# Performance work log

Hardware: AMD Instinct MI355X
Metric: run time of the kernel (lower is better)

The kernel has to match this reference:

```python
import jax, jax.numpy as jnp
import numpy as np


def _bilinear_sample(fea, gx, gy):
    """grid_sample, bilinear, zero padding, align_corners=True.
    fea: [B,C,H,W]; gx, gy: [B,N] normalized coords in [-1,1]. Returns [B,N,C]."""
    B, C, H, W = fea.shape
    feaT = fea.transpose(0, 2, 3, 1)  # [B,H,W,C]
    x = (gx + 1.0) * ((W - 1) * 0.5)
    y = (gy + 1.0) * ((H - 1) * 0.5)
    x0 = jnp.floor(x)
    y0 = jnp.floor(y)
    bidx = jnp.arange(B)[:, None]
    out = jnp.zeros(gx.shape + (C,), fea.dtype)
    for dx, dy in ((0, 0), (1, 0), (0, 1), (1, 1)):
        xi = x0 + dx
        yi = y0 + dy
        w = (1.0 - jnp.abs(x - xi)) * (1.0 - jnp.abs(y - yi))
        valid = (xi >= 0) & (xi <= W - 1) & (yi >= 0) & (yi <= H - 1)
        xic = jnp.clip(xi, 0, W - 1).astype(jnp.int32)
        yic = jnp.clip(yi, 0, H - 1).astype(jnp.int32)
        vals = feaT[bidx, yic, xic]  # [B,N,C]
        out = out + (w * valid.astype(fea.dtype))[:, :, None] * vals
    return out


def _homo_warping(src_fea, src_proj, ref_proj, depth_values):
    """src_fea [B,C,H,W]; src_proj/ref_proj [B,4,4]; depth_values [B,D,H,W].
    Returns warped volume [B,C,D,H,W]."""
    B, C, H, W = src_fea.shape
    D = depth_values.shape[1]
    proj = jnp.einsum('bij,bjk->bik', src_proj, jnp.linalg.inv(ref_proj))
    rot = proj[:, :3, :3]
    trans = proj[:, :3, 3]
    ys, xs = jnp.meshgrid(jnp.arange(H, dtype=src_fea.dtype),
                          jnp.arange(W, dtype=src_fea.dtype), indexing='ij')
    xyz = jnp.stack([xs.ravel(), ys.ravel(), jnp.ones(H * W, src_fea.dtype)], 0)  # [3,HW]
    rot_xyz = jnp.einsum('bij,jn->bin', rot, xyz)  # [B,3,HW]
    d = depth_values.reshape(B, 1, D, H * W)
    pxyz = rot_xyz[:, :, None, :] * d + trans[:, :, None, None]  # [B,3,D,HW]
    z = pxyz[:, 2]
    gx = pxyz[:, 0] / z
    gy = pxyz[:, 1] / z
    nx = gx / ((W - 1) * 0.5) - 1.0
    ny = gy / ((H - 1) * 0.5) - 1.0
    sampled = _bilinear_sample(src_fea, nx.reshape(B, -1), ny.reshape(B, -1))  # [B,D*H*W,C]
    return sampled.reshape(B, D, H, W, C).transpose(0, 4, 1, 2, 3)


def _combine_proj(proj):
    """proj [B,2,4,4]: [:,0]=extrinsic 4x4, [:,1,:3,:3]=intrinsic. Returns [B,4,4]."""
    upd = jnp.einsum('bij,bjk->bik', proj[:, 1, :3, :3], proj[:, 0, :3, :4])
    return proj[:, 0].at[:, :3, :4].set(upd)


def setup_inputs() -> dict:
    B, V, C, H, W, D = 2, 5, 32, 256, 320, 4
    key = jax.random.key(0)
    feats = jax.random.normal(key, (B, V, C, H, W), dtype=jnp.float32)
    rng = np.random.default_rng(0)
    K = np.eye(4, dtype=np.float32)
    K[0, 0] = 0.9 * W; K[1, 1] = 0.9 * W; K[0, 2] = W / 2.0; K[1, 2] = H / 2.0
    projs = np.zeros((B, V, 2, 4, 4), dtype=np.float32)
    for b in range(B):
        for v in range(V):
            ang = 0.0 if v == 0 else float(rng.uniform(-0.05, 0.05))
            ca, sa = np.cos(ang), np.sin(ang)
            E = np.eye(4, dtype=np.float32)
            E[:3, :3] = np.array([[ca, 0, sa], [0, 1, 0], [-sa, 0, ca]], dtype=np.float32)
            if v > 0:
                E[:3, 3] = rng.uniform(-20, 20, size=3).astype(np.float32)
            projs[b, v, 0] = E
            projs[b, v, 1] = K
    dmin, dmax = 425.0, 935.0
    base = np.linspace(dmin, dmax, D, dtype=np.float32)
    depth = np.broadcast_to(base[None, :, None, None], (B, D, H, W)).copy()
    depth += rng.uniform(-5, 5, size=(B, D, H, W)).astype(np.float32)
    return {'feats': feats,
            'proj_matrices': jnp.asarray(projs),
            'depth_values': jnp.asarray(depth)}


def reference(feats, proj_matrices, depth_values):
    """HAMMER.get_volume_variance_and_mask.
    feats [B,V,C,H,W], proj_matrices [B,V,2,4,4], depth_values [B,D,H,W].
    Returns (volume_variance [B,C,D,H,W], cv_mask [B,H,W])."""
    B, V, C, H, W = feats.shape
    D = depth_values.shape[1]
    ref_proj = _combine_proj(proj_matrices[:, 0])
    ref_vol = jnp.broadcast_to(feats[:, 0, :, None], (B, C, D, H, W))
    vol_sum = ref_vol
    vol_sq = ref_vol ** 2
    cv_mask = jnp.zeros((B, H, W), feats.dtype)
    for v in range(1, V):
        src_proj = _combine_proj(proj_matrices[:, v])
        warped = _homo_warping(feats[:, v], src_proj, ref_proj, depth_values)
        cv_mask = cv_mask + jnp.count_nonzero(
            jnp.count_nonzero(warped, axis=1), axis=1).astype(feats.dtype)
        vol_sum = vol_sum + warped
        vol_sq = vol_sq + warped ** 2
    inv_v = 1.0 / V
    volume_variance = vol_sq * inv_v - (vol_sum * inv_v) ** 2
    return volume_variance, cv_mask
```

## Files before the change

kernel.cpp:

```cpp
#include <hip/hip_runtime.h>

constexpr int B = 2, V = 5, C = 32, H = 256, W = 320, D = 4;
constexpr int HW = H * W;

__device__ float g_rt[B * (V - 1) * 12];

__device__ void combine_np(const float* __restrict__ proj, int b, int v, float Mo[4][4]) {
    const float* E = proj + ((size_t)(b * V + v) * 2 + 0) * 16;
    const float* K = proj + ((size_t)(b * V + v) * 2 + 1) * 16;
    for (int i = 0; i < 3; i++)
        for (int j = 0; j < 4; j++) {
            float acc = __fadd_rn(0.0f, __fmul_rn(K[i * 4 + 0], E[0 * 4 + j]));
            acc = __fadd_rn(acc, __fmul_rn(K[i * 4 + 1], E[1 * 4 + j]));
            acc = __fadd_rn(acc, __fmul_rn(K[i * 4 + 2], E[2 * 4 + j]));
            Mo[i][j] = acc;
        }
    for (int j = 0; j < 4; j++) Mo[3][j] = E[3 * 4 + j];
}

__global__ void setup_proj(const float* __restrict__ proj) {
    int t = threadIdx.x;
    if (t >= B * (V - 1)) return;
    int b = t / (V - 1);
    int v = t % (V - 1) + 1;

    float R[4][4], S[4][4];
    combine_np(proj, b, 0, R);
    combine_np(proj, b, v, S);

    float I4[4][4];
    for (int i = 0; i < 4; i++)
        for (int j = 0; j < 4; j++) I4[i][j] = 0.0f;

    float d0 = __fdiv_rn(1.0f, R[0][0]);
    I4[0][0] = d0;
    float d1 = __fdiv_rn(1.0f, R[1][1]);
    I4[1][1] = d1;
    {
        float x0 = R[0][1];
        if (x0 != 0.0f) x0 = __fmul_rn(x0, I4[0][0]);
        I4[0][1] = __fmul_rn(x0, -d1);
    }
    float d2 = __fdiv_rn(1.0f, R[2][2]);
    I4[2][2] = d2;
    {
        float x0 = R[0][2], x1 = R[1][2];
        if (x0 != 0.0f) x0 = __fmul_rn(x0, I4[0][0]);
        if (x1 != 0.0f) {
            x0 = __fadd_rn(x0, __fmul_rn(x1, I4[0][1]));
            x1 = __fmul_rn(x1, I4[1][1]);
        }
        I4[0][2] = __fmul_rn(x0, -d2);
        I4[1][2] = __fmul_rn(x1, -d2);
    }
    float d3 = __fdiv_rn(1.0f, R[3][3]);
    I4[3][3] = d3;
    {
        float x0 = R[0][3], x1 = R[1][3], x2 = R[2][3];
        if (x0 != 0.0f) x0 = __fmul_rn(x0, I4[0][0]);
        if (x1 != 0.0f) {
            x0 = __fadd_rn(x0, __fmul_rn(x1, I4[0][1]));
            x1 = __fmul_rn(x1, I4[1][1]);
        }
        if (x2 != 0.0f) {
            x0 = __fadd_rn(x0, __fmul_rn(x2, I4[0][2]));
            x1 = __fadd_rn(x1, __fmul_rn(x2, I4[1][2]));
            x2 = __fmul_rn(x2, I4[2][2]);
        }
        I4[0][3] = __fmul_rn(x0, -d3);
        I4[1][3] = __fmul_rn(x1, -d3);
        I4[2][3] = __fmul_rn(x2, -d3);
    }

    float P[3][4];
    for (int i = 0; i < 3; i++)
        for (int k = 0; k < 4; k++) {
            float acc = 0.0f;
            for (int j = 0; j < 4; j++)
                acc = __fadd_rn(acc, __fmul_rn(S[i][j], I4[j][k]));
            P[i][k] = acc;
        }

    float* out = g_rt + t * 12;
    out[0] = P[0][0]; out[1] = P[0][1]; out[2] = P[0][2];
    out[3] = P[1][0]; out[4] = P[1][1]; out[5] = P[1][2];
    out[6] = P[2][0]; out[7] = P[2][1]; out[8] = P[2][2];
    out[9] = P[0][3]; out[10] = P[1][3]; out[11] = P[2][3];
}

__global__ __launch_bounds__(256) void warp_var(
    const float* __restrict__ feats,
    const float* __restrict__ depthv,
    float* __restrict__ var_out,
    float* __restrict__ mask_out)
{
    int idx = blockIdx.x * 256 + threadIdx.x;
    int w = idx % W;
    int h = (idx / W) % H;
    int d = (idx / HW) % D;
    int b = idx / (HW * D);

    float depth = depthv[idx];

    const float xf = (float)w, yf = (float)h;
    const float hwX = 0.5f * (float)(W - 1);
    const float hwY = 0.5f * (float)(H - 1);
    const float rcpX = 1.0f / 159.5f;
    const float rcpY = 1.0f / 127.5f;

    int   toff[V - 1][4];
    float twt[V - 1][4];

#pragma unroll
    for (int v = 1; v < V; v++) {
        const float* P = g_rt + ((size_t)b * (V - 1) + (v - 1)) * 12;
        float rx = __fadd_rn(__fmaf_rn(P[1], yf, __fmul_rn(P[0], xf)), P[2]);
        float ry = __fadd_rn(__fmaf_rn(P[4], yf, __fmul_rn(P[3], xf)), P[5]);
        float rz = __fadd_rn(__fmaf_rn(P[7], yf, __fmul_rn(P[6], xf)), P[8]);
        float px = __fadd_rn(__fmul_rn(rx, depth), P[9]);
        float py = __fadd_rn(__fmul_rn(ry, depth), P[10]);
        float pz = __fadd_rn(__fmul_rn(rz, depth), P[11]);
        float gx = __fdiv_rn(px, pz);
        float gy = __fdiv_rn(py, pz);
        float nx = __fadd_rn(__fmul_rn(gx, rcpX), -1.0f);
        float ny = __fadd_rn(__fmul_rn(gy, rcpY), -1.0f);
        float x = __fmul_rn(__fadd_rn(nx, 1.0f), hwX);
        float y = __fmul_rn(__fadd_rn(ny, 1.0f), hwY);

        float x0 = floorf(x), y0 = floorf(y);
        float x1 = x0 + 1.0f, y1 = y0 + 1.0f;

        float wx0 = __fadd_rn(1.0f, -fabsf(__fadd_rn(x, -x0)));
        float wx1 = __fadd_rn(1.0f, -fabsf(__fadd_rn(x, -x1)));
        float wy0 = __fadd_rn(1.0f, -fabsf(__fadd_rn(y, -y0)));
        float wy1 = __fadd_rn(1.0f, -fabsf(__fadd_rn(y, -y1)));

        float vx0 = (x0 >= 0.0f && x0 <= (float)(W - 1)) ? 1.0f : 0.0f;
        float vx1 = (x1 >= 0.0f && x1 <= (float)(W - 1)) ? 1.0f : 0.0f;
        float vy0 = (y0 >= 0.0f && y0 <= (float)(H - 1)) ? 1.0f : 0.0f;
        float vy1 = (y1 >= 0.0f && y1 <= (float)(H - 1)) ? 1.0f : 0.0f;

        float s00 = __fmul_rn(__fmul_rn(wx0, wy0), __fmul_rn(vx0, vy0));
        float s10 = __fmul_rn(__fmul_rn(wx1, wy0), __fmul_rn(vx1, vy0));
        float s01 = __fmul_rn(__fmul_rn(wx0, wy1), __fmul_rn(vx0, vy1));
        float s11 = __fmul_rn(__fmul_rn(wx1, wy1), __fmul_rn(vx1, vy1));

        int xi0 = (int)fminf(fmaxf(x0, 0.0f), (float)(W - 1));
        int xi1 = (int)fminf(fmaxf(x1, 0.0f), (float)(W - 1));
        int yi0 = (int)fminf(fmaxf(y0, 0.0f), (float)(H - 1));
        int yi1 = (int)fminf(fmaxf(y1, 0.0f), (float)(H - 1));

        int vb = (b * V + v) * C * HW;
        toff[v - 1][0] = vb + yi0 * W + xi0;
        toff[v - 1][1] = vb + yi0 * W + xi1;
        toff[v - 1][2] = vb + yi1 * W + xi0;
        toff[v - 1][3] = vb + yi1 * W + xi1;
        twt[v - 1][0] = s00;
        twt[v - 1][1] = s10;
        twt[v - 1][2] = s01;
        twt[v - 1][3] = s11;
    }

    const int rb = b * V * C * HW + h * W + w;
    const float inv_v = 1.0f / (float)V;
    const size_t obase = ((size_t)b * C * D + d) * HW + (size_t)h * W + w;

    int nzmask = 0;

#pragma unroll 2
    for (int c = 0; c < C; c++) {
        const int cofs = c * HW;
        float rv = feats[rb + cofs];
        float s = rv;
        float q = rv * rv;
#pragma unroll
        for (int v = 0; v < V - 1; v++) {
            float f00 = feats[toff[v][0] + cofs];
            float f10 = feats[toff[v][1] + cofs];
            float f01 = feats[toff[v][2] + cofs];
            float f11 = feats[toff[v][3] + cofs];
            float val = twt[v][0] * f00 + twt[v][1] * f10 + twt[v][2] * f01 + twt[v][3] * f11;
            nzmask |= (val != 0.0f) ? (1 << v) : 0;
            s += val;
            q += val * val;
        }
        float sm = s * inv_v;
        float vv = q * inv_v - sm * sm;
        __builtin_nontemporal_store(vv, &var_out[obase + (size_t)c * (D * HW)]);
    }

    float maskc = (float)__popc(nzmask);
    atomicAdd(&mask_out[(size_t)b * HW + (size_t)h * W + w], maskc);
}

extern "C" void kernel_launch(void* const* d_in, const int* in_sizes, int n_in,
                              void* d_out, int out_size, void* d_ws, size_t ws_size,
                              hipStream_t stream) {
    const float* feats = (const float*)d_in[0];
    const float* proj = (const float*)d_in[1];
    const float* depthv = (const float*)d_in[2];

    float* var = (float*)d_out;
    float* mask = var + (size_t)B * C * D * HW;

    hipMemsetAsync(mask, 0, sizeof(float) * (size_t)B * HW, stream);

    setup_proj<<<1, 64, 0, stream>>>(proj);

    int n = B * D * HW;
    warp_var<<<n / 256, 256, 0, stream>>>(feats, depthv, var, mask);
}
```

Before: 277.7 us.

## Process all depth planes per thread and drop mask atomics

Each thread now handles one pixel across all depth hypotheses, so the reference feature value is loaded once per channel instead of once per depth. The mask is computed fully per thread and written directly, which removes the memset and the atomic adds. Block size drops to 128 and a block-index swizzle is added. Per-thread register state grows sharply because offsets and weights are kept for all view-depth pairs, which risks spills and lower occupancy.

```diff
diff --git a/kernel.cpp b/kernel.cpp
--- a/kernel.cpp
+++ b/kernel.cpp
@@ -2,6 +2,9 @@
 
 constexpr int B = 2, V = 5, C = 32, H = 256, W = 320, D = 4;
 constexpr int HW = H * W;
+constexpr int NTHREAD = B * HW;
+constexpr int BLK = 128;
+constexpr int NBLK = NTHREAD / BLK;
 
 __device__ float g_rt[B * (V - 1) * 12];
 
@@ -88,19 +91,25 @@
     out[9] = P[0][3]; out[10] = P[1][3]; out[11] = P[2][3];
 }
 
-__global__ __launch_bounds__(256) void warp_var(
+__global__ __launch_bounds__(BLK, 2) void warp_var(
     const float* __restrict__ feats,
     const float* __restrict__ depthv,
     float* __restrict__ var_out,
     float* __restrict__ mask_out)
 {
-    int idx = blockIdx.x * 256 + threadIdx.x;
-    int w = idx % W;
-    int h = (idx / W) % H;
-    int d = (idx / HW) % D;
-    int b = idx / (HW * D);
-
-    float depth = depthv[idx];
+    int bid = blockIdx.x;
+    int bswz = (bid & 7) * (NBLK / 8) + (bid >> 3);
+    int idx = bswz * BLK + threadIdx.x;
+
+    int hw = idx % HW;
+    int b = idx / HW;
+    int w = hw % W;
+    int h = hw / W;
+
+    float dep[D];
+#pragma unroll
+    for (int d = 0; d < D; d++)
+        dep[d] = depthv[(size_t)(b * D + d) * HW + hw];
 
     const float xf = (float)w, yf = (float)h;
     const float hwX = 0.5f * (float)(W - 1);
@@ -108,8 +117,8 @@
     const float rcpX = 1.0f / 159.5f;
     const float rcpY = 1.0f / 127.5f;
 
-    int   toff[V - 1][4];
-    float twt[V - 1][4];
+    int   toff[(V - 1) * D][4];
+    float twt[(V - 1) * D][4];
 
 #pragma unroll
     for (int v = 1; v < V; v++) {
@@ -117,80 +126,90 @@
         float rx = __fadd_rn(__fmaf_rn(P[1], yf, __fmul_rn(P[0], xf)), P[2]);
         float ry = __fadd_rn(__fmaf_rn(P[4], yf, __fmul_rn(P[3], xf)), P[5]);
         float rz = __fadd_rn(__fmaf_rn(P[7], yf, __fmul_rn(P[6], xf)), P[8]);
-        float px = __fadd_rn(__fmul_rn(rx, depth), P[9]);
-        float py = __fadd_rn(__fmul_rn(ry, depth), P[10]);
-        float pz = __fadd_rn(__fmul_rn(rz, depth), P[11]);
-        float gx = __fdiv_rn(px, pz);
-        float gy = __fdiv_rn(py, pz);
-        float nx = __fadd_rn(__fmul_rn(gx, rcpX), -1.0f);
-        float ny = __fadd_rn(__fmul_rn(gy, rcpY), -1.0f);
-        float x = __fmul_rn(__fadd_rn(nx, 1.0f), hwX);
-        float y = __fmul_rn(__fadd_rn(ny, 1.0f), hwY);
-
-        float x0 = floorf(x), y0 = floorf(y);
-        float x1 = x0 + 1.0f, y1 = y0 + 1.0f;
-
-        float wx0 = __fadd_rn(1.0f, -fabsf(__fadd_rn(x, -x0)));
-        float wx1 = __fadd_rn(1.0f, -fabsf(__fadd_rn(x, -x1)));
-        float wy0 = __fadd_rn(1.0f, -fabsf(__fadd_rn(y, -y0)));
-        float wy1 = __fadd_rn(1.0f, -fabsf(__fadd_rn(y, -y1)));
-
-        float vx0 = (x0 >= 0.0f && x0 <= (float)(W - 1)) ? 1.0f : 0.0f;
-        float vx1 = (x1 >= 0.0f && x1 <= (float)(W - 1)) ? 1.0f : 0.0f;
-        float vy0 = (y0 >= 0.0f && y0 <= (float)(H - 1)) ? 1.0f : 0.0f;
-        float vy1 = (y1 >= 0.0f && y1 <= (float)(H - 1)) ? 1.0f : 0.0f;
-
-        float s00 = __fmul_rn(__fmul_rn(wx0, wy0), __fmul_rn(vx0, vy0));
-        float s10 = __fmul_rn(__fmul_rn(wx1, wy0), __fmul_rn(vx1, vy0));
-        float s01 = __fmul_rn(__fmul_rn(wx0, wy1), __fmul_rn(vx0, vy1));
-        float s11 = __fmul_rn(__fmul_rn(wx1, wy1), __fmul_rn(vx1, vy1));
-
-        int xi0 = (int)fminf(fmaxf(x0, 0.0f), (float)(W - 1));
-        int xi1 = (int)fminf(fmaxf(x1, 0.0f), (float)(W - 1));
-        int yi0 = (int)fminf(fmaxf(y0, 0.0f), (float)(H - 1));
-        int yi1 = (int)fminf(fmaxf(y1, 0.0f), (float)(H - 1));
-
-        int vb = (b * V + v) * C * HW;
-        toff[v - 1][0] = vb + yi0 * W + xi0;
-        toff[v - 1][1] = vb + yi0 * W + xi1;
-        toff[v - 1][2] = vb + yi1 * W + xi0;
-        toff[v - 1][3] = vb + yi1 * W + xi1;
-        twt[v - 1][0] = s00;
-        twt[v - 1][1] = s10;
-        twt[v - 1][2] = s01;
-        twt[v - 1][3] = s11;
-    }
-
-    const int rb = b * V * C * HW + h * W + w;
+        const int vb = (b * V + v) * C * HW;
+#pragma unroll
+        for (int d = 0; d < D; d++) {
+            const int p = (v - 1) * D + d;
+            float px = __fadd_rn(__fmul_rn(rx, dep[d]), P[9]);
+            float py = __fadd_rn(__fmul_rn(ry, dep[d]), P[10]);
+            float pz = __fadd_rn(__fmul_rn(rz, dep[d]), P[11]);
+            float gx = __fdiv_rn(px, pz);
+            float gy = __fdiv_rn(py, pz);
+            float nx = __fadd_rn(__fmul_rn(gx, rcpX), -1.0f);
+            float ny = __fadd_rn(__fmul_rn(gy, rcpY), -1.0f);
+            float x = __fmul_rn(__fadd_rn(nx, 1.0f), hwX);
+            float y = __fmul_rn(__fadd_rn(ny, 1.0f), hwY);
+
+            float x0 = floorf(x), y0 = floorf(y);
+            float x1 = x0 + 1.0f, y1 = y0 + 1.0f;
+
+            float wx0 = __fadd_rn(1.0f, -fabsf(__fadd_rn(x, -x0)));
+            float wx1 = __fadd_rn(1.0f, -fabsf(__fadd_rn(x, -x1)));
+            float wy0 = __fadd_rn(1.0f, -fabsf(__fadd_rn(y, -y0)));
+            float wy1 = __fadd_rn(1.0f, -fabsf(__fadd_rn(y, -y1)));
+
+            float vx0 = (x0 >= 0.0f && x0 <= (float)(W - 1)) ? 1.0f : 0.0f;
+            float vx1 = (x1 >= 0.0f && x1 <= (float)(W - 1)) ? 1.0f : 0.0f;
+            float vy0 = (y0 >= 0.0f && y0 <= (float)(H - 1)) ? 1.0f : 0.0f;
+            float vy1 = (y1 >= 0.0f && y1 <= (float)(H - 1)) ? 1.0f : 0.0f;
+
+            twt[p][0] = __fmul_rn(__fmul_rn(wx0, wy0), __fmul_rn(vx0, vy0));
+            twt[p][1] = __fmul_rn(__fmul_rn(wx1, wy0), __fmul_rn(vx1, vy0));
+            twt[p][2] = __fmul_rn(__fmul_rn(wx0, wy1), __fmul_rn(vx0, vy1));
+            twt[p][3] = __fmul_rn(__fmul_rn(wx1, wy1), __fmul_rn(vx1, vy1));
+
+            int xi0 = (int)fminf(fmaxf(x0, 0.0f), (float)(W - 1));
+            int xi1 = (int)fminf(fmaxf(x1, 0.0f), (float)(W - 1));
+            int yi0 = (int)fminf(fmaxf(y0, 0.0f), (float)(H - 1));
+            int yi1 = (int)fminf(fmaxf(y1, 0.0f), (float)(H - 1));
+
+            toff[p][0] = vb + yi0 * W + xi0;
+            toff[p][1] = vb + yi0 * W + xi1;
+            toff[p][2] = vb + yi1 * W + xi0;
+            toff[p][3] = vb + yi1 * W + xi1;
+        }
+    }
+
+    const int rb = b * V * C * HW + hw;
     const float inv_v = 1.0f / (float)V;
-    const size_t obase = ((size_t)b * C * D + d) * HW + (size_t)h * W + w;
+    const size_t obase = (size_t)b * C * D * HW + (size_t)hw;
 
     int nzmask = 0;
 
-#pragma unroll 2
     for (int c = 0; c < C; c++) {
         const int cofs = c * HW;
         float rv = feats[rb + cofs];
-        float s = rv;
-        float q = rv * rv;
+        float s[D], q[D];
+#pragma unroll
+        for (int d = 0; d < D; d++) {
+            s[d] = rv;
+            q[d] = rv * rv;
+        }
 #pragma unroll
         for (int v = 0; v < V - 1; v++) {
-            float f00 = feats[toff[v][0] + cofs];
-            float f10 = feats[toff[v][1] + cofs];
-            float f01 = feats[toff[v][2] + cofs];
-            float f11 = feats[toff[v][3] + cofs];
-            float val = twt[v][0] * f00 + twt[v][1] * f10 + twt[v][2] * f01 + twt[v][3] * f11;
-            nzmask |= (val != 0.0f) ? (1 << v) : 0;
-            s += val;
-            q += val * val;
-        }
-        float sm = s * inv_v;
-        float vv = q * inv_v - sm * sm;
-        __builtin_nontemporal_store(vv, &var_out[obase + (size_t)c * (D * HW)]);
-    }
-
-    float maskc = (float)__popc(nzmask);
-    atomicAdd(&mask_out[(size_t)b * HW + (size_t)h * W + w], maskc);
+#pragma unroll
+            for (int d = 0; d < D; d++) {
+                const int p = v * D + d;
+                float f00 = feats[toff[p][0] + cofs];
+                float f10 = feats[toff[p][1] + cofs];
+                float f01 = feats[toff[p][2] + cofs];
+                float f11 = feats[toff[p][3] + cofs];
+                float val = twt[p][0] * f00 + twt[p][1] * f10 + twt[p][2] * f01 + twt[p][3] * f11;
+                nzmask |= (val != 0.0f) ? (1 << p) : 0;
+                s[d] += val;
+                q[d] += val * val;
+            }
+        }
+#pragma unroll
+        for (int d = 0; d < D; d++) {
+            float sm = s[d] * inv_v;
+            float vv = q[d] * inv_v - sm * sm;
+            __builtin_nontemporal_store(
+                vv, &var_out[obase + (size_t)c * (D * HW) + (size_t)d * HW]);
+        }
+    }
+
+    mask_out[(size_t)b * HW + hw] = (float)__popc(nzmask);
 }
 
 extern "C" void kernel_launch(void* const* d_in, const int* in_sizes, int n_in,
@@ -203,10 +222,7 @@
     float* var = (float*)d_out;
     float* mask = var + (size_t)B * C * D * HW;
 
-    hipMemsetAsync(mask, 0, sizeof(float) * (size_t)B * HW, stream);
-
     setup_proj<<<1, 64, 0, stream>>>(proj);
 
-    int n = B * D * HW;
-    warp_var<<<n / 256, 256, 0, stream>>>(feats, depthv, var, mask);
-}
+    warp_var<<<NBLK, BLK, 0, stream>>>(feats, depthv, var, mask);
+}
```

Measured after the change: 299.5 us. +7.9%, slower.

## Interleave depth planes per thread group, swizzle blocks, reduce mask via shuffles

Applied to the files above, without the earlier changes.

Changes the thread-to-work mapping so that the four depth samples of each pixel sit in adjacent lanes, and remaps block IDs with a swizzle over eight groups. The per-pixel count mask is then reduced across the four lanes with shuffles and written directly. This removes the atomics and the memset launch. Adjacent lanes now share reference-feature loads and likely nearby gather addresses. The cost is that output stores and depth loads become strided across the four lanes instead of fully coalesced.

```diff
diff --git a/kernel.cpp b/kernel.cpp
--- a/kernel.cpp
+++ b/kernel.cpp
@@ -2,6 +2,9 @@
 
 constexpr int B = 2, V = 5, C = 32, H = 256, W = 320, D = 4;
 constexpr int HW = H * W;
+constexpr int NTHREAD = B * HW * D;
+constexpr int BLK = 256;
+constexpr int NBLK = NTHREAD / BLK;
 
 __device__ float g_rt[B * (V - 1) * 12];
 
@@ -94,13 +97,18 @@
     float* __restrict__ var_out,
     float* __restrict__ mask_out)
 {
-    int idx = blockIdx.x * 256 + threadIdx.x;
-    int w = idx % W;
-    int h = (idx / W) % H;
-    int d = (idx / HW) % D;
-    int b = idx / (HW * D);
-
-    float depth = depthv[idx];
+    int bid = blockIdx.x;
+    int bswz = (bid & 7) * (NBLK / 8) + (bid >> 3);
+    int t = bswz * BLK + threadIdx.x;
+
+    int d = t & 3;
+    int p = t >> 2;
+    int hw = p % HW;
+    int b = p / HW;
+    int w = hw % W;
+    int h = hw / W;
+
+    float depth = depthv[(size_t)(b * D + d) * HW + hw];
 
     const float xf = (float)w, yf = (float)h;
     const float hwX = 0.5f * (float)(W - 1);
@@ -140,10 +148,10 @@
         float vy0 = (y0 >= 0.0f && y0 <= (float)(H - 1)) ? 1.0f : 0.0f;
         float vy1 = (y1 >= 0.0f && y1 <= (float)(H - 1)) ? 1.0f : 0.0f;
 
-        float s00 = __fmul_rn(__fmul_rn(wx0, wy0), __fmul_rn(vx0, vy0));
-        float s10 = __fmul_rn(__fmul_rn(wx1, wy0), __fmul_rn(vx1, vy0));
-        float s01 = __fmul_rn(__fmul_rn(wx0, wy1), __fmul_rn(vx0, vy1));
-        float s11 = __fmul_rn(__fmul_rn(wx1, wy1), __fmul_rn(vx1, vy1));
+        twt[v - 1][0] = __fmul_rn(__fmul_rn(wx0, wy0), __fmul_rn(vx0, vy0));
+        twt[v - 1][1] = __fmul_rn(__fmul_rn(wx1, wy0), __fmul_rn(vx1, vy0));
+        twt[v - 1][2] = __fmul_rn(__fmul_rn(wx0, wy1), __fmul_rn(vx0, vy1));
+        twt[v - 1][3] = __fmul_rn(__fmul_rn(wx1, wy1), __fmul_rn(vx1, vy1));
 
         int xi0 = (int)fminf(fmaxf(x0, 0.0f), (float)(W - 1));
         int xi1 = (int)fminf(fmaxf(x1, 0.0f), (float)(W - 1));
@@ -155,15 +163,11 @@
         toff[v - 1][1] = vb + yi0 * W + xi1;
         toff[v - 1][2] = vb + yi1 * W + xi0;
         toff[v - 1][3] = vb + yi1 * W + xi1;
-        twt[v - 1][0] = s00;
-        twt[v - 1][1] = s10;
-        twt[v - 1][2] = s01;
-        twt[v - 1][3] = s11;
-    }
-
-    const int rb = b * V * C * HW + h * W + w;
+    }
+
+    const int rb = b * V * C * HW + hw;
     const float inv_v = 1.0f / (float)V;
-    const size_t obase = ((size_t)b * C * D + d) * HW + (size_t)h * W + w;
+    const size_t obase = ((size_t)b * C * D + d) * HW + (size_t)hw;
 
     int nzmask = 0;
 
@@ -189,8 +193,10 @@
         __builtin_nontemporal_store(vv, &var_out[obase + (size_t)c * (D * HW)]);
     }
 
-    float maskc = (float)__popc(nzmask);
-    atomicAdd(&mask_out[(size_t)b * HW + (size_t)h * W + w], maskc);
+    int m = __popc(nzmask);
+    m += __shfl_xor(m, 1);
+    m += __shfl_xor(m, 2);
+    if (d == 0) mask_out[(size_t)b * HW + hw] = (float)m;
 }
 
 extern "C" void kernel_launch(void* const* d_in, const int* in_sizes, int n_in,
@@ -203,10 +209,7 @@
     float* var = (float*)d_out;
     float* mask = var + (size_t)B * C * D * HW;
 
-    hipMemsetAsync(mask, 0, sizeof(float) * (size_t)B * HW, stream);
-
     setup_proj<<<1, 64, 0, stream>>>(proj);
 
-    int n = B * D * HW;
-    warp_var<<<n / 256, 256, 0, stream>>>(feats, depthv, var, mask);
-}
+    warp_var<<<NBLK, BLK, 0, stream>>>(feats, depthv, var, mask);
+}
```

Result: slower. 360.2 us (+29.7%).
